# Kernel tuning notes

Measured on AMD Instinct MI355X. Metric: run time of the kernel, lower is better.

## Reference

```python
import jax, jax.numpy as jnp
import numpy as np

N_NODES = 100000
N_EDGES = 1600000
IN_DIM = 128
OUT_DIM = 64


def setup_inputs() -> dict:
    key = jax.random.key(0)
    k1, k2, k3 = jax.random.split(key, 3)
    x = jax.random.normal(k1, (N_NODES, IN_DIM), dtype=jnp.float32)
    edge_index = jax.random.randint(k2, (2, N_EDGES), 0, N_NODES, dtype=jnp.int64)
    W = jax.random.normal(k3, (IN_DIM, OUT_DIM), dtype=jnp.float32) * (1.0 / np.sqrt(IN_DIM))
    b = jnp.zeros((OUT_DIM,), dtype=jnp.float32)
    return {"x": x, "edge_index": edge_index, "W": W, "b": b}


def reference(x, edge_index, W, b):
    row = edge_index[0]  # source nodes
    col = edge_index[1]  # target nodes (aggregation index)
    n = x.shape[0]

    # gcn_norm with add_self_loops=False: degree from edge weights (ones) at target
    ones = jnp.ones((edge_index.shape[1],), dtype=x.dtype)
    deg = jax.ops.segment_sum(ones, col, num_segments=n)  # [N]
    deg_inv_sqrt = jnp.where(deg > 0, jax.lax.rsqrt(jnp.maximum(deg, 1e-12)), 0.0)
    norm = deg_inv_sqrt[row] * deg_inv_sqrt[col]  # [E]

    # linear transform first (bias added after aggregation, as in PyG GCNConv)
    h = x @ W  # [N, OUT_DIM]

    # gather source features, scale by norm, scatter-add to targets
    msg = h[row] * norm[:, None]  # [E, OUT_DIM]
    out = jax.ops.segment_sum(msg, col, num_segments=n) + b  # [N, OUT_DIM]

    return jax.nn.relu(out)
```

## Files before the change

kernel.cpp:

```cpp
#include <hip/hip_runtime.h>
#include <hip/hip_bf16.h>

#define IN_DIM 128
#define OUT_DIM 64
#define NPB_LOG 7
#define NPB (1 << NPB_LOG)
#define MAXBUCK 1024
#define B1 512
#define CAP 4096

static inline size_t align_up(size_t v, size_t a) { return (v + a - 1) & ~(a - 1); }

__device__ __forceinline__ unsigned short f2bf(float f) {
    unsigned int x = __float_as_uint(f);
    unsigned int r = (x + 0x7fffu + ((x >> 16) & 1u)) >> 16;
    return (unsigned short)r;
}

typedef _Float16 half8 __attribute__((ext_vector_type(8)));
typedef float f32x4 __attribute__((ext_vector_type(4)));

__global__ void __launch_bounds__(256) kA_ticket(
    const int* __restrict__ col, int* __restrict__ BinTotal,
    int* __restrict__ tickets, int n_edges, int nbuck, int chunk) {
    __shared__ int hist[MAXBUCK];
    int t = threadIdx.x;
    for (int i = t; i < nbuck; i += 256) hist[i] = 0;
    __syncthreads();
    int start = blockIdx.x * chunk;
    int end = min(n_edges, start + chunk);
    for (int i = start + t; i < end; i += 256)
        atomicAdd(&hist[col[i] >> NPB_LOG], 1);
    __syncthreads();
    int* trow = tickets + (size_t)blockIdx.x * nbuck;
    for (int i = t; i < nbuck; i += 256)
        trow[i] = atomicAdd(&BinTotal[i], hist[i]);
}

__global__ void __launch_bounds__(256) kS2_scantotals(
    const int* __restrict__ BinTotal, int* __restrict__ BucketStart,
    int nbuck, int n_edges) {
    __shared__ int s[256];
    int t = threadIdx.x;
    int v[4];
#pragma unroll
    for (int j = 0; j < 4; ++j) {
        int idx = t * 4 + j;
        v[j] = (idx < nbuck) ? BinTotal[idx] : 0;
    }
    int tsum = v[0] + v[1] + v[2] + v[3];
    s[t] = tsum;
    __syncthreads();
    for (int off = 1; off < 256; off <<= 1) {
        int x = (t >= off) ? s[t - off] : 0;
        __syncthreads();
        s[t] += x;
        __syncthreads();
    }
    int run = s[t] - tsum;
#pragma unroll
    for (int j = 0; j < 4; ++j) {
        int idx = t * 4 + j;
        if (idx < nbuck) BucketStart[idx] = run;
        run += v[j];
    }
    if (t == 0) BucketStart[nbuck] = n_edges;
}

__global__ void __launch_bounds__(256) kB_scatter(
    const int* __restrict__ row, const int* __restrict__ col,
    const int* __restrict__ BucketStart, const int* __restrict__ tickets,
    unsigned int* __restrict__ EdgeBuf, int n_edges, int nbuck, int chunk) {
    __shared__ int cur[MAXBUCK];
    const int* trow = tickets + (size_t)blockIdx.x * nbuck;
    int t = threadIdx.x;
    for (int i = t; i < nbuck; i += 256)
        cur[i] = BucketStart[i] + trow[i];
    __syncthreads();
    int start = blockIdx.x * chunk;
    int end = min(n_edges, start + chunk);
    for (int i = start + t; i < end; i += 256) {
        int c = col[i];
        int r = row[i];
        int bin = c >> NPB_LOG;
        int p = atomicAdd(&cur[bin], 1);
        EdgeBuf[p] = ((unsigned int)r << NPB_LOG) | (unsigned int)(c & (NPB - 1));
    }
}

__global__ void __launch_bounds__(256) kD_degree(
    const unsigned int* __restrict__ EdgeBuf, const int* __restrict__ BucketStart,
    float* __restrict__ dis, int n_nodes) {
    __shared__ int cnt[NPB];
    int t = threadIdx.x;
    if (t < NPB) cnt[t] = 0;
    __syncthreads();
    int es = BucketStart[blockIdx.x];
    int ee = BucketStart[blockIdx.x + 1];
    for (int i = es + t; i < ee; i += 256)
        atomicAdd(&cnt[EdgeBuf[i] & (NPB - 1)], 1);
    __syncthreads();
    int nb0 = blockIdx.x << NPB_LOG;
    if (t < NPB) {
        int node = nb0 + t;
        if (node < n_nodes) {
            int d = cnt[t];
            dis[node] = (d > 0) ? rsqrtf((float)d) : 0.0f;
        }
    }
}

__global__ void __launch_bounds__(256) k_matmul_mfma(
    const float* __restrict__ x, const float* __restrict__ W,
    const float* __restrict__ dis, unsigned short* __restrict__ h, int n_nodes) {
    const int lane = threadIdx.x & 63;
    const int m = lane & 15;
    const int q = lane >> 4;
    const int wid = (blockIdx.x * blockDim.x + threadIdx.x) >> 6;
    const int ntiles = (n_nodes + 15) >> 4;
    if (wid >= ntiles) return;

    half8 bfrag[4][4];
#pragma unroll
    for (int kt = 0; kt < 4; ++kt) {
#pragma unroll
        for (int nt = 0; nt < 4; ++nt) {
            int k0 = kt * 32 + q * 8;
            int c = nt * 16 + m;
#pragma unroll
            for (int j = 0; j < 8; ++j)
                bfrag[kt][nt][j] = (_Float16)W[(size_t)(k0 + j) * OUT_DIM + c];
        }
    }

    const int nb = wid << 4;
    int arow = nb + m;
    if (arow >= n_nodes) arow = n_nodes - 1;
    const float* xr = x + (size_t)arow * IN_DIM;

    f32x4 acc[4];
#pragma unroll
    for (int nt = 0; nt < 4; ++nt) acc[nt] = (f32x4){0.f, 0.f, 0.f, 0.f};

#pragma unroll
    for (int kt = 0; kt < 4; ++kt) {
        const float4* xp = (const float4*)(xr + kt * 32 + q * 8);
        float4 lo = xp[0];
        float4 hi = xp[1];
        half8 afrag;
        afrag[0] = (_Float16)lo.x; afrag[1] = (_Float16)lo.y;
        afrag[2] = (_Float16)lo.z; afrag[3] = (_Float16)lo.w;
        afrag[4] = (_Float16)hi.x; afrag[5] = (_Float16)hi.y;
        afrag[6] = (_Float16)hi.z; afrag[7] = (_Float16)hi.w;
#pragma unroll
        for (int nt = 0; nt < 4; ++nt)
            acc[nt] = __builtin_amdgcn_mfma_f32_16x16x32_f16(afrag, bfrag[kt][nt],
                                                             acc[nt], 0, 0, 0);
    }

#pragma unroll
    for (int r = 0; r < 4; ++r) {
        int node = nb + q * 4 + r;
        if (node < n_nodes) {
            float dv = dis[node];
            unsigned short* hp = h + (size_t)node * OUT_DIM + m;
#pragma unroll
            for (int nt = 0; nt < 4; ++nt)
                hp[nt * 16] = f2bf(acc[nt][r] * dv);
        }
    }
}

__global__ void __launch_bounds__(512) kF_sortagg(
    const unsigned int* __restrict__ EdgeBuf, const int* __restrict__ BucketStart,
    const float* __restrict__ dis, const unsigned short* __restrict__ h,
    const float* __restrict__ b, float* __restrict__ out,
    int* __restrict__ edge_src, int n_nodes) {
    __shared__ int cnt[NPB];
    __shared__ int seg[NPB];
    __shared__ int cursor[NPB];
    __shared__ int sbuf[CAP];
    int t = threadIdx.x;
    int es = BucketStart[blockIdx.x];
    int ee = BucketStart[blockIdx.x + 1];
    int ne = ee - es;
    int nb0 = blockIdx.x << NPB_LOG;

    if (t < NPB) cnt[t] = 0;
    __syncthreads();
    for (int i = es + t; i < ee; i += 512)
        atomicAdd(&cnt[EdgeBuf[i] & (NPB - 1)], 1);
    __syncthreads();

    if (t < NPB) seg[t] = cnt[t];
    __syncthreads();
    for (int off = 1; off < NPB; off <<= 1) {
        int x = 0;
        if (t < NPB && t >= off) x = seg[t - off];
        __syncthreads();
        if (t < NPB) seg[t] += x;
        __syncthreads();
    }
    if (t < NPB) cursor[t] = seg[t] - cnt[t];
    __syncthreads();

    const int lane = t & 63;
    const int wv = t >> 6;
    const int quarter = lane >> 4;
    const int qlane = lane & 15;
    float4 bias = ((const float4*)b)[qlane];

    if (ne <= CAP) {
        for (int i = es + t; i < ee; i += 512) {
            unsigned int v = EdgeBuf[i];
            int c = (int)(v & (NPB - 1));
            int p = atomicAdd(&cursor[c], 1);
            sbuf[p] = (int)(v >> NPB_LOG);
        }
        __syncthreads();

        for (int nl = wv; nl < NPB; nl += 8) {
            int node = nb0 + nl;
            if (node >= n_nodes) break;
            int e_ = seg[nl];
            int s_ = e_ - cnt[nl];
            float a0 = 0.f, a1 = 0.f, a2 = 0.f, a3 = 0.f;
            for (int j0 = s_; j0 < e_; j0 += 8) {
                int iA = j0 + quarter;
                int iB = j0 + quarter + 4;
                int rA = sbuf[iA < e_ ? iA : s_];
                int rB = sbuf[iB < e_ ? iB : s_];
                uint2 vA = make_uint2(0u, 0u), vB = make_uint2(0u, 0u);
                if (iA < e_)
                    vA = *(const uint2*)(h + (size_t)rA * OUT_DIM + qlane * 4);
                if (iB < e_)
                    vB = *(const uint2*)(h + (size_t)rB * OUT_DIM + qlane * 4);
                a0 += __uint_as_float(vA.x << 16);
                a1 += __uint_as_float(vA.x & 0xFFFF0000u);
                a2 += __uint_as_float(vA.y << 16);
                a3 += __uint_as_float(vA.y & 0xFFFF0000u);
                a0 += __uint_as_float(vB.x << 16);
                a1 += __uint_as_float(vB.x & 0xFFFF0000u);
                a2 += __uint_as_float(vB.y << 16);
                a3 += __uint_as_float(vB.y & 0xFFFF0000u);
            }
            a0 += __shfl_xor(a0, 16, 64); a0 += __shfl_xor(a0, 32, 64);
            a1 += __shfl_xor(a1, 16, 64); a1 += __shfl_xor(a1, 32, 64);
            a2 += __shfl_xor(a2, 16, 64); a2 += __shfl_xor(a2, 32, 64);
            a3 += __shfl_xor(a3, 16, 64); a3 += __shfl_xor(a3, 32, 64);
            if (quarter == 0) {
                float dv = dis[node];
                float4 o;
                o.x = fmaxf(fmaf(a0, dv, bias.x), 0.f);
                o.y = fmaxf(fmaf(a1, dv, bias.y), 0.f);
                o.z = fmaxf(fmaf(a2, dv, bias.z), 0.f);
                o.w = fmaxf(fmaf(a3, dv, bias.w), 0.f);
                ((float4*)(out + (size_t)node * OUT_DIM))[qlane] = o;
            }
        }
    } else {
        for (int i = es + t; i < ee; i += 512) {
            unsigned int v = EdgeBuf[i];
            int c = (int)(v & (NPB - 1));
            int p = atomicAdd(&cursor[c], 1);
            edge_src[es + p] = (int)(v >> NPB_LOG);
        }
        __threadfence();
        __syncthreads();
        for (int nl = wv; nl < NPB; nl += 8) {
            int node = nb0 + nl;
            if (node >= n_nodes) break;
            int e_ = seg[nl];
            int s_ = e_ - cnt[nl];
            float a0 = 0.f, a1 = 0.f, a2 = 0.f, a3 = 0.f;
            for (int j0 = s_; j0 < e_; j0 += 8) {
                int iA = j0 + quarter;
                int iB = j0 + quarter + 4;
                int rA = edge_src[es + (iA < e_ ? iA : s_)];
                int rB = edge_src[es + (iB < e_ ? iB : s_)];
                uint2 vA = make_uint2(0u, 0u), vB = make_uint2(0u, 0u);
                if (iA < e_)
                    vA = *(const uint2*)(h + (size_t)rA * OUT_DIM + qlane * 4);
                if (iB < e_)
                    vB = *(const uint2*)(h + (size_t)rB * OUT_DIM + qlane * 4);
                a0 += __uint_as_float(vA.x << 16);
                a1 += __uint_as_float(vA.x & 0xFFFF0000u);
                a2 += __uint_as_float(vA.y << 16);
                a3 += __uint_as_float(vA.y & 0xFFFF0000u);
                a0 += __uint_as_float(vB.x << 16);
                a1 += __uint_as_float(vB.x & 0xFFFF0000u);
                a2 += __uint_as_float(vB.y << 16);
                a3 += __uint_as_float(vB.y & 0xFFFF0000u);
            }
            a0 += __shfl_xor(a0, 16, 64); a0 += __shfl_xor(a0, 32, 64);
            a1 += __shfl_xor(a1, 16, 64); a1 += __shfl_xor(a1, 32, 64);
            a2 += __shfl_xor(a2, 16, 64); a2 += __shfl_xor(a2, 32, 64);
            a3 += __shfl_xor(a3, 16, 64); a3 += __shfl_xor(a3, 32, 64);
            if (quarter == 0) {
                float dv = dis[node];
                float4 o;
                o.x = fmaxf(fmaf(a0, dv, bias.x), 0.f);
                o.y = fmaxf(fmaf(a1, dv, bias.y), 0.f);
                o.z = fmaxf(fmaf(a2, dv, bias.z), 0.f);
                o.w = fmaxf(fmaf(a3, dv, bias.w), 0.f);
                ((float4*)(out + (size_t)node * OUT_DIM))[qlane] = o;
            }
        }
    }
}

#define MM_NODES 16
__global__ void __launch_bounds__(256) k_matmul_f32(
    const float* __restrict__ x, const float* __restrict__ W,
    const float* __restrict__ dis, float* __restrict__ h, int n_nodes) {
    __shared__ float xs[MM_NODES * IN_DIM];
    const int lane = threadIdx.x & 63;
    const int wv = threadIdx.x >> 6;
    float w[IN_DIM];
#pragma unroll
    for (int k = 0; k < IN_DIM; ++k) w[k] = W[k * OUT_DIM + lane];
    int nchunks = (n_nodes + MM_NODES - 1) / MM_NODES;
    for (int ch = blockIdx.x; ch < nchunks; ch += gridDim.x) {
        int base = ch * MM_NODES;
        int nrows = min(MM_NODES, n_nodes - base);
        __syncthreads();
        const float4* xg = (const float4*)(x + (size_t)base * IN_DIM);
        int nf4 = nrows * IN_DIM / 4;
        for (int i = threadIdx.x; i < nf4; i += 256) ((float4*)xs)[i] = xg[i];
        __syncthreads();
#pragma unroll
        for (int j = 0; j < 4; ++j) {
            int local = wv * 4 + j;
            int node = base + local;
            if (local < nrows) {
                const float4* xr = (const float4*)(xs + local * IN_DIM);
                float acc = 0.0f;
#pragma unroll
                for (int k4 = 0; k4 < IN_DIM / 4; ++k4) {
                    float4 xv = xr[k4];
                    acc = fmaf(xv.x, w[k4 * 4 + 0], acc);
                    acc = fmaf(xv.y, w[k4 * 4 + 1], acc);
                    acc = fmaf(xv.z, w[k4 * 4 + 2], acc);
                    acc = fmaf(xv.w, w[k4 * 4 + 3], acc);
                }
                h[(size_t)node * OUT_DIM + lane] = acc * dis[node];
            }
        }
    }
}

__global__ void k_degree_fb(const int* __restrict__ col, int* __restrict__ deg,
                            int n_edges) {
    int i = blockIdx.x * blockDim.x + threadIdx.x;
    int stride = gridDim.x * blockDim.x;
    for (; i < n_edges; i += stride) atomicAdd(&deg[col[i]], 1);
}

__global__ void k_rsqrt_fb(const int* __restrict__ deg, float* __restrict__ dis, int n) {
    int i = blockIdx.x * blockDim.x + threadIdx.x;
    if (i < n) {
        int d = deg[i];
        dis[i] = (d > 0) ? rsqrtf((float)d) : 0.0f;
    }
}

__global__ void __launch_bounds__(256) k_scatter_fb(
    const int* __restrict__ row, const int* __restrict__ col,
    const float* __restrict__ dis, const float* __restrict__ h,
    float* __restrict__ out, int n_edges) {
    const int lane = threadIdx.x & 63;
    int e = (blockIdx.x * blockDim.x + threadIdx.x) >> 6;
    int nw = (gridDim.x * blockDim.x) >> 6;
    for (; e < n_edges; e += nw) {
        int r = row[e];
        int c = col[e];
        float v = h[(size_t)r * OUT_DIM + lane] * dis[c];
        atomicAdd(&out[(size_t)c * OUT_DIM + lane], v);
    }
}

__global__ void k_bias_relu_fb(float* __restrict__ out, const float* __restrict__ b,
                               int total) {
    int i = blockIdx.x * blockDim.x + threadIdx.x;
    int stride = gridDim.x * blockDim.x;
    for (; i < total; i += stride) {
        float v = out[i] + b[i & (OUT_DIM - 1)];
        out[i] = fmaxf(v, 0.0f);
    }
}

extern "C" void kernel_launch(void* const* d_in, const int* in_sizes, int n_in,
                              void* d_out, int out_size, void* d_ws, size_t ws_size,
                              hipStream_t stream) {
    const float* x = (const float*)d_in[0];
    const int* ei = (const int*)d_in[1];
    const float* W = (const float*)d_in[2];
    const float* b = (const float*)d_in[3];
    float* out = (float*)d_out;

    const int n_nodes = in_sizes[0] / IN_DIM;
    const int n_edges = in_sizes[1] / 2;
    const int* row = ei;
    const int* col = ei + n_edges;

    const int nbuck = (n_nodes + NPB - 1) >> NPB_LOG;
    const int chunk = (n_edges + B1 - 1) / B1;

    char* wsb = (char*)d_ws;
    size_t off = 0;
    int* BinTotal = (int*)(wsb + off);   off += align_up((size_t)nbuck * 4, 256);
    int* BucketStart = (int*)(wsb + off);off += align_up((size_t)(nbuck + 1) * 4, 256);
    int* tickets = (int*)(wsb + off);    off += align_up((size_t)B1 * nbuck * 4, 256);
    float* dis = (float*)(wsb + off);    off += align_up((size_t)n_nodes * 4, 256);
    unsigned int* EdgeBuf = (unsigned int*)(wsb + off);
                                         off += align_up((size_t)n_edges * 4, 256);
    int* edge_src = (int*)(wsb + off);   off += align_up((size_t)n_edges * 4, 256);
    unsigned short* h = (unsigned short*)(wsb + off);
                                         off += (size_t)n_nodes * OUT_DIM * 2;
    const size_t needed = off;

    const bool ok = (ws_size >= needed) && (nbuck <= MAXBUCK) &&
                    (n_nodes <= (1 << 24));

    if (ok) {
        hipMemsetAsync(BinTotal, 0, (size_t)nbuck * 4, stream);
        kA_ticket<<<B1, 256, 0, stream>>>(col, BinTotal, tickets, n_edges, nbuck,
                                          chunk);
        kS2_scantotals<<<1, 256, 0, stream>>>(BinTotal, BucketStart, nbuck, n_edges);
        kB_scatter<<<B1, 256, 0, stream>>>(row, col, BucketStart, tickets, EdgeBuf,
                                           n_edges, nbuck, chunk);
        kD_degree<<<nbuck, 256, 0, stream>>>(EdgeBuf, BucketStart, dis, n_nodes);
        int ntiles = (n_nodes + 15) / 16;
        int mm_blocks = (ntiles + 3) / 4;
        k_matmul_mfma<<<mm_blocks, 256, 0, stream>>>(x, W, dis, h, n_nodes);
        kF_sortagg<<<nbuck, 512, 0, stream>>>(EdgeBuf, BucketStart, dis, h, b,
                                              out, edge_src, n_nodes);
    } else {
        char* p = (char*)d_ws;
        int* deg_f = (int*)p;
        float* dis_f = (float*)(p + align_up((size_t)n_nodes * 4, 256));
        float* h_f = (float*)(p + 2 * align_up((size_t)n_nodes * 4, 256));
        hipMemsetAsync(deg_f, 0, (size_t)n_nodes * 4, stream);
        hipMemsetAsync(out, 0, (size_t)out_size * 4, stream);
        k_degree_fb<<<1024, 256, 0, stream>>>(col, deg_f, n_edges);
        k_rsqrt_fb<<<(n_nodes + 255) / 256, 256, 0, stream>>>(deg_f, dis_f, n_nodes);
        k_matmul_f32<<<1024, 256, 0, stream>>>(x, W, dis_f, h_f, n_nodes);
        k_scatter_fb<<<2048, 256, 0, stream>>>(row, col, dis_f, h_f, out, n_edges);
        k_bias_relu_fb<<<2048, 256, 0, stream>>>(out, b, n_nodes * OUT_DIM);
    }
}
```

Before: 198.2 us.

## Use coarse 512-node buckets for edge binning with fine 128-node aggregation sub-blocks

Edge binning now uses coarse buckets of 512 target nodes, so there are four times fewer bins, and the ticket and scatter passes use half as many blocks. This shrinks the tickets array and the per-block histogram work. The aggregation kernel still runs one block per 128 nodes, but each block scans its whole parent coarse bucket and filters for its own sub-range. That means EdgeBuf is read four times per coarse bucket. Oversized sub-buckets now spill into a compact buffer allocated through a global atomic cursor.

```diff
diff --git a/kernel.cpp b/kernel.cpp
--- a/kernel.cpp
+++ b/kernel.cpp
@@ -3,10 +3,12 @@
 
 #define IN_DIM 128
 #define OUT_DIM 64
-#define NPB_LOG 7
-#define NPB (1 << NPB_LOG)
-#define MAXBUCK 1024
-#define B1 512
+#define CLOG 9
+#define CNPB (1 << CLOG)
+#define FLOG 7
+#define FNPB (1 << FLOG)
+#define MAXCOARSE 1024
+#define B1 256
 #define CAP 4096
 
 static inline size_t align_up(size_t v, size_t a) { return (v + a - 1) & ~(a - 1); }
@@ -23,14 +25,14 @@
 __global__ void __launch_bounds__(256) kA_ticket(
     const int* __restrict__ col, int* __restrict__ BinTotal,
     int* __restrict__ tickets, int n_edges, int nbuck, int chunk) {
-    __shared__ int hist[MAXBUCK];
+    __shared__ int hist[MAXCOARSE];
     int t = threadIdx.x;
     for (int i = t; i < nbuck; i += 256) hist[i] = 0;
     __syncthreads();
     int start = blockIdx.x * chunk;
     int end = min(n_edges, start + chunk);
     for (int i = start + t; i < end; i += 256)
-        atomicAdd(&hist[col[i] >> NPB_LOG], 1);
+        atomicAdd(&hist[col[i] >> CLOG], 1);
     __syncthreads();
     int* trow = tickets + (size_t)blockIdx.x * nbuck;
     for (int i = t; i < nbuck; i += 256)
@@ -71,7 +73,7 @@
     const int* __restrict__ row, const int* __restrict__ col,
     const int* __restrict__ BucketStart, const int* __restrict__ tickets,
     unsigned int* __restrict__ EdgeBuf, int n_edges, int nbuck, int chunk) {
-    __shared__ int cur[MAXBUCK];
+    __shared__ int cur[MAXCOARSE];
     const int* trow = tickets + (size_t)blockIdx.x * nbuck;
     int t = threadIdx.x;
     for (int i = t; i < nbuck; i += 256)
@@ -82,29 +84,29 @@
     for (int i = start + t; i < end; i += 256) {
         int c = col[i];
         int r = row[i];
-        int bin = c >> NPB_LOG;
+        int bin = c >> CLOG;
         int p = atomicAdd(&cur[bin], 1);
-        EdgeBuf[p] = ((unsigned int)r << NPB_LOG) | (unsigned int)(c & (NPB - 1));
+        EdgeBuf[p] = ((unsigned int)r << CLOG) | (unsigned int)(c & (CNPB - 1));
     }
 }
 
 __global__ void __launch_bounds__(256) kD_degree(
     const unsigned int* __restrict__ EdgeBuf, const int* __restrict__ BucketStart,
     float* __restrict__ dis, int n_nodes) {
-    __shared__ int cnt[NPB];
+    __shared__ int cnt[CNPB];
     int t = threadIdx.x;
-    if (t < NPB) cnt[t] = 0;
+    for (int i = t; i < CNPB; i += 256) cnt[i] = 0;
     __syncthreads();
     int es = BucketStart[blockIdx.x];
     int ee = BucketStart[blockIdx.x + 1];
     for (int i = es + t; i < ee; i += 256)
-        atomicAdd(&cnt[EdgeBuf[i] & (NPB - 1)], 1);
-    __syncthreads();
-    int nb0 = blockIdx.x << NPB_LOG;
-    if (t < NPB) {
-        int node = nb0 + t;
+        atomicAdd(&cnt[EdgeBuf[i] & (CNPB - 1)], 1);
+    __syncthreads();
+    int nb0 = blockIdx.x << CLOG;
+    for (int i = t; i < CNPB; i += 256) {
+        int node = nb0 + i;
         if (node < n_nodes) {
-            int d = cnt[t];
+            int d = cnt[i];
             dis[node] = (d > 0) ? rsqrtf((float)d) : 0.0f;
         }
     }
@@ -175,33 +177,42 @@
     const unsigned int* __restrict__ EdgeBuf, const int* __restrict__ BucketStart,
     const float* __restrict__ dis, const unsigned short* __restrict__ h,
     const float* __restrict__ b, float* __restrict__ out,
-    int* __restrict__ edge_src, int n_nodes) {
-    __shared__ int cnt[NPB];
-    __shared__ int seg[NPB];
-    __shared__ int cursor[NPB];
+    int* __restrict__ spill, int* __restrict__ spillcur, int n_nodes) {
+    __shared__ int cnt[FNPB];
+    __shared__ int seg[FNPB];
+    __shared__ int cursor[FNPB];
     __shared__ int sbuf[CAP];
+    __shared__ int sbase_sh;
     int t = threadIdx.x;
-    int es = BucketStart[blockIdx.x];
-    int ee = BucketStart[blockIdx.x + 1];
-    int ne = ee - es;
-    int nb0 = blockIdx.x << NPB_LOG;
-
-    if (t < NPB) cnt[t] = 0;
-    __syncthreads();
-    for (int i = es + t; i < ee; i += 512)
-        atomicAdd(&cnt[EdgeBuf[i] & (NPB - 1)], 1);
-    __syncthreads();
-
-    if (t < NPB) seg[t] = cnt[t];
-    __syncthreads();
-    for (int off = 1; off < NPB; off <<= 1) {
+    int parent = blockIdx.x >> 2;
+    int sub = blockIdx.x & 3;
+    int es = BucketStart[parent];
+    int ee = BucketStart[parent + 1];
+    int nb0 = blockIdx.x << FLOG;
+
+    if (t < FNPB) cnt[t] = 0;
+    __syncthreads();
+    for (int i = es + t; i < ee; i += 512) {
+        unsigned int v = EdgeBuf[i];
+        if ((int)((v >> FLOG) & 3u) == sub)
+            atomicAdd(&cnt[v & (FNPB - 1)], 1);
+    }
+    __syncthreads();
+
+    if (t < FNPB) seg[t] = cnt[t];
+    __syncthreads();
+    for (int off = 1; off < FNPB; off <<= 1) {
         int x = 0;
-        if (t < NPB && t >= off) x = seg[t - off];
-        __syncthreads();
-        if (t < NPB) seg[t] += x;
-        __syncthreads();
-    }
-    if (t < NPB) cursor[t] = seg[t] - cnt[t];
+        if (t < FNPB && t >= off) x = seg[t - off];
+        __syncthreads();
+        if (t < FNPB) seg[t] += x;
+        __syncthreads();
+    }
+    if (t < FNPB) cursor[t] = seg[t] - cnt[t];
+    __syncthreads();
+
+    int ne_f = seg[FNPB - 1];
+    if (t == 0 && ne_f > CAP) sbase_sh = atomicAdd(spillcur, ne_f);
     __syncthreads();
 
     const int lane = t & 63;
@@ -210,16 +221,17 @@
     const int qlane = lane & 15;
     float4 bias = ((const float4*)b)[qlane];
 
-    if (ne <= CAP) {
+    if (ne_f <= CAP) {
         for (int i = es + t; i < ee; i += 512) {
             unsigned int v = EdgeBuf[i];
-            int c = (int)(v & (NPB - 1));
-            int p = atomicAdd(&cursor[c], 1);
-            sbuf[p] = (int)(v >> NPB_LOG);
-        }
-        __syncthreads();
-
-        for (int nl = wv; nl < NPB; nl += 8) {
+            if ((int)((v >> FLOG) & 3u) == sub) {
+                int p = atomicAdd(&cursor[v & (FNPB - 1)], 1);
+                sbuf[p] = (int)(v >> CLOG);
+            }
+        }
+        __syncthreads();
+
+        for (int nl = wv; nl < FNPB; nl += 8) {
             int node = nb0 + nl;
             if (node >= n_nodes) break;
             int e_ = seg[nl];
@@ -259,15 +271,17 @@
             }
         }
     } else {
+        int sbase = sbase_sh;
         for (int i = es + t; i < ee; i += 512) {
             unsigned int v = EdgeBuf[i];
-            int c = (int)(v & (NPB - 1));
-            int p = atomicAdd(&cursor[c], 1);
-            edge_src[es + p] = (int)(v >> NPB_LOG);
+            if ((int)((v >> FLOG) & 3u) == sub) {
+                int p = atomicAdd(&cursor[v & (FNPB - 1)], 1);
+                spill[sbase + p] = (int)(v >> CLOG);
+            }
         }
         __threadfence();
         __syncthreads();
-        for (int nl = wv; nl < NPB; nl += 8) {
+        for (int nl = wv; nl < FNPB; nl += 8) {
             int node = nb0 + nl;
             if (node >= n_nodes) break;
             int e_ = seg[nl];
@@ -276,8 +290,8 @@
             for (int j0 = s_; j0 < e_; j0 += 8) {
                 int iA = j0 + quarter;
                 int iB = j0 + quarter + 4;
-                int rA = edge_src[es + (iA < e_ ? iA : s_)];
-                int rB = edge_src[es + (iB < e_ ? iB : s_)];
+                int rA = spill[sbase + (iA < e_ ? iA : s_)];
+                int rB = spill[sbase + (iB < e_ ? iB : s_)];
                 uint2 vA = make_uint2(0u, 0u), vB = make_uint2(0u, 0u);
                 if (iA < e_)
                     vA = *(const uint2*)(h + (size_t)rA * OUT_DIM + qlane * 4);
@@ -403,38 +417,40 @@
     const int* row = ei;
     const int* col = ei + n_edges;
 
-    const int nbuck = (n_nodes + NPB - 1) >> NPB_LOG;
+    const int nbc = (n_nodes + CNPB - 1) >> CLOG;
+    const int nbf = (n_nodes + FNPB - 1) >> FLOG;
     const int chunk = (n_edges + B1 - 1) / B1;
 
     char* wsb = (char*)d_ws;
     size_t off = 0;
-    int* BinTotal = (int*)(wsb + off);   off += align_up((size_t)nbuck * 4, 256);
-    int* BucketStart = (int*)(wsb + off);off += align_up((size_t)(nbuck + 1) * 4, 256);
-    int* tickets = (int*)(wsb + off);    off += align_up((size_t)B1 * nbuck * 4, 256);
+    int* BinTotal = (int*)(wsb + off);   off += align_up((size_t)(nbc + 8) * 4, 256);
+    int* spillcur = BinTotal + nbc;
+    int* BucketStart = (int*)(wsb + off);off += align_up((size_t)(nbc + 1) * 4, 256);
+    int* tickets = (int*)(wsb + off);    off += align_up((size_t)B1 * nbc * 4, 256);
     float* dis = (float*)(wsb + off);    off += align_up((size_t)n_nodes * 4, 256);
     unsigned int* EdgeBuf = (unsigned int*)(wsb + off);
                                          off += align_up((size_t)n_edges * 4, 256);
-    int* edge_src = (int*)(wsb + off);   off += align_up((size_t)n_edges * 4, 256);
+    int* spill = (int*)(wsb + off);      off += align_up((size_t)n_edges * 4, 256);
     unsigned short* h = (unsigned short*)(wsb + off);
                                          off += (size_t)n_nodes * OUT_DIM * 2;
     const size_t needed = off;
 
-    const bool ok = (ws_size >= needed) && (nbuck <= MAXBUCK) &&
-                    (n_nodes <= (1 << 24));
+    const bool ok = (ws_size >= needed) && (nbc <= MAXCOARSE) &&
+                    (n_nodes <= (1 << 22));
 
     if (ok) {
-        hipMemsetAsync(BinTotal, 0, (size_t)nbuck * 4, stream);
-        kA_ticket<<<B1, 256, 0, stream>>>(col, BinTotal, tickets, n_edges, nbuck,
+        hipMemsetAsync(BinTotal, 0, (size_t)(nbc + 8) * 4, stream);
+        kA_ticket<<<B1, 256, 0, stream>>>(col, BinTotal, tickets, n_edges, nbc,
                                           chunk);
-        kS2_scantotals<<<1, 256, 0, stream>>>(BinTotal, BucketStart, nbuck, n_edges);
+        kS2_scantotals<<<1, 256, 0, stream>>>(BinTotal, BucketStart, nbc, n_edges);
         kB_scatter<<<B1, 256, 0, stream>>>(row, col, BucketStart, tickets, EdgeBuf,
-                                           n_edges, nbuck, chunk);
-        kD_degree<<<nbuck, 256, 0, stream>>>(EdgeBuf, BucketStart, dis, n_nodes);
+                                           n_edges, nbc, chunk);
+        kD_degree<<<nbc, 256, 0, stream>>>(EdgeBuf, BucketStart, dis, n_nodes);
         int ntiles = (n_nodes + 15) / 16;
         int mm_blocks = (ntiles + 3) / 4;
         k_matmul_mfma<<<mm_blocks, 256, 0, stream>>>(x, W, dis, h, n_nodes);
-        kF_sortagg<<<nbuck, 512, 0, stream>>>(EdgeBuf, BucketStart, dis, h, b,
-                                              out, edge_src, n_nodes);
+        kF_sortagg<<<nbf, 512, 0, stream>>>(EdgeBuf, BucketStart, dis, h, b,
+                                            out, spill, spillcur, n_nodes);
     } else {
         char* p = (char*)d_ws;
         int* deg_f = (int*)p;
```

Result: faster. 193.3 us (-2.5%).
